# Performance work log

Hardware: AMD Instinct MI355X
Metric: run time of the kernel (lower is better)

The kernel has to match this reference:

```python
import jax, jax.numpy as jnp
import numpy as np

B, C, HZ, HX = 32, 256, 13, 25

# ---------- basic layers ----------

def _conv1x1(x, w, b):
    # x: [B,Cin,H,W], w: [Cout,Cin]
    return jnp.einsum('bchw,oc->bohw', x, w) + b[None, :, None, None]

def _conv2d(x, w, b, pad):
    y = jax.lax.conv_general_dilated(x, w, (1, 1), [(pad, pad), (pad, pad)],
                                     dimension_numbers=('NCHW', 'OIHW', 'NCHW'))
    return y + b[None, :, None, None]

def _bn(x, gamma, beta, mean, var):
    # eval-mode batchnorm with running stats, eps=1e-5 (torch default)
    s = gamma / jnp.sqrt(var + 1e-5)
    return x * s[None, :, None, None] + (beta - mean * s)[None, :, None, None]

def _gelu(x):
    return jax.nn.gelu(x, approximate=False)  # torch nn.GELU default = exact erf

# ---------- sparsemax (softThresholdingOperation) ----------
# The torch topk version recursively refines unresolved rows with 2*topk; since
# 2*128>=169 and 2*512>=625 it is mathematically exact sparsemax here.

def _sparsemax_impl(s):
    s = s - jnp.max(s, axis=-1, keepdims=True)
    d = s.shape[-1]
    z = -jnp.sort(-s, axis=-1)                      # descending sort
    cs = jnp.cumsum(z, axis=-1) - 1.0
    k = jnp.arange(1, d + 1, dtype=s.dtype)
    support = k * z > cs
    supp = jnp.sum(support, axis=-1, keepdims=True)  # int support size
    tau = jnp.take_along_axis(cs, supp - 1, axis=-1) / supp.astype(s.dtype)
    out = jnp.maximum(s - tau, 0.0)
    return out, (out, supp)

@jax.custom_vjp
def sparsemax(s):
    return _sparsemax_impl(s)[0]

def _sm_fwd(s):
    return _sparsemax_impl(s)

def _sm_bwd(res, g):
    out, supp = res
    gi = jnp.where(out != 0, g, 0.0)
    v_hat = jnp.sum(gi, axis=-1, keepdims=True) / supp.astype(out.dtype)
    return (jnp.where(out != 0, gi - v_hat, gi),)

sparsemax.defvjp(_sm_fwd, _sm_bwd)

# ---------- connected components + fill holes (GPU-native, no scipy) ----------

def _dilate8_max(lab):
    # 3x3 max-pool label propagation (8-connectivity, matches np.ones((3,3)))
    Bb, H, W = lab.shape
    p = jnp.pad(lab, ((0, 0), (1, 1), (1, 1)))
    shifts = [p[:, i:i + H, j:j + W] for i in range(3) for j in range(3)]
    return jnp.max(jnp.stack(shifts, 0), 0)

def _dilate4_or(x):
    # cross-shaped binary dilation (4-connectivity, scipy fill_holes default)
    Bb, H, W = x.shape
    p = jnp.pad(x, ((0, 0), (1, 1), (1, 1)))
    return (p[:, 1:H + 1, 1:W + 1] | p[:, 0:H, 1:W + 1] | p[:, 2:H + 2, 1:W + 1]
            | p[:, 1:H + 1, 0:W] | p[:, 1:H + 1, 2:W + 2])

def _largest_cc_filled(m):
    # m: bool [B,H,W] -> float mask of largest 8-connected component, holes filled
    Bb, H, W = m.shape
    HW = H * W
    idx = jnp.arange(1, HW + 1, dtype=jnp.int32).reshape(1, H, W)
    lab0 = jnp.where(m, idx, 0)

    def body(st):
        lab, _ = st
        return (jnp.where(m, _dilate8_max(lab), 0), lab)

    lab = jax.lax.while_loop(lambda st: jnp.any(st[0] != st[1]), body,
                             (lab0, -jnp.ones_like(lab0)))[0]

    counts = jax.vmap(lambda l, mm: jnp.zeros(HW + 1, jnp.int32)
                      .at[l.ravel()].add(mm.ravel()))(lab, m.astype(jnp.int32))
    largest = jnp.argmax(counts.at[:, 0].set(-1), axis=-1).astype(jnp.int32)
    comp = (lab == largest[:, None, None]) & m

    # fill holes: flood-fill background (4-conn) from the border, invert
    bg = ~comp
    border = jnp.zeros((H, W), bool).at[0].set(True).at[-1].set(True) \
        .at[:, 0].set(True).at[:, -1].set(True)
    seed = bg & border[None]

    def body2(st):
        r, _ = st
        return (bg & _dilate4_or(r), r)

    reach = jax.lax.while_loop(lambda st: jnp.any(st[0] != st[1]), body2,
                               (seed, jnp.zeros_like(seed)))[0]
    return ~reach

# ---------- module forward ----------

def _forward(zf, xf, sup_w, sup_b, sup_gamma, sup_beta, sup_mean, sup_var,
             q_w, q_b, q_gamma, q_beta, q_mean, q_var,
             g_w1, g_b1, g_w2, g_b2, g_gamma, g_beta, g_mean, g_var,
             fi_w, fi_b, fi_gamma, fi_beta, fi_mean, fi_var,
             fi1_w, fi1_b, fi1_gamma, fi1_beta, fi1_mean, fi1_var):
    Bb, Cc, Hz, Wz = zf.shape
    _, _, Hx, Wx = xf.shape

    xf_trans = _gelu(_bn(_conv1x1(xf, q_w, q_b), q_gamma, q_beta, q_mean, q_var))
    zf_trans = _gelu(_bn(_conv1x1(zf, sup_w, sup_b), sup_gamma, sup_beta, sup_mean, sup_var))
    xf_g = _gelu(_bn(_conv1x1(_conv2d(xf, g_w1, g_b1, 1), g_w2, g_b2),
                     g_gamma, g_beta, g_mean, g_var))

    zt = zf_trans.reshape(Bb, Cc, Hz * Wz)
    xt = xf_trans.reshape(Bb, Cc, Hx * Wx)
    zp = zf.reshape(Bb, Cc, Hz * Wz)
    xp = xf.reshape(Bb, Cc, Hx * Wx)

    zf_s = sparsemax(jnp.einsum('bcn,bcm->bnm', zt, zt))      # [B,169,169]
    zp = zp + jnp.einsum('bcn,bnm->bcm', zp, zf_s)

    si = sparsemax(jnp.einsum('bcn,bcm->bnm', zp, xp))         # [B,169,625]
    si2 = sparsemax(jnp.einsum('bcn,bcm->bnm', zp, xt))
    si = si + si2

    mask2 = jax.lax.stop_gradient(jnp.mean(si2, axis=1)) != 0  # [B,625]
    mask = _largest_cc_filled(mask2.reshape(Bb, Hx, Wx)).astype(xf.dtype)[:, None]

    si_img = si.reshape(Bb, Hz * Wz, Hx, Wx)                   # [B,169,25,25]
    fi_out = _gelu(_bn(_conv1x1(si_img, fi_w, fi_b), fi_gamma, fi_beta, fi_mean, fi_var))
    concat = jnp.concatenate([fi_out, xf_g * mask], axis=1)
    return _gelu(_bn(_conv2d(concat, fi1_w, fi1_b, 2),
                     fi1_gamma, fi1_beta, fi1_mean, fi1_var))

# ---------- setup ----------

def setup_inputs() -> dict:
    key = jax.random.key(0)
    ks = jax.random.split(key, 40)
    f32 = jnp.float32

    def n(k, shape, s=0.05):
        return (jax.random.normal(k, shape) * s).astype(f32)

    inp = {}
    inp['zf'] = jax.random.normal(ks[0], (B, C, HZ, HZ), f32)
    inp['xf'] = jax.random.normal(ks[1], (B, C, HX, HX), f32)

    def bn_params(pfx, k0):
        inp[pfx + '_gamma'] = (1.0 + n(ks[k0], (C,))).astype(f32)
        inp[pfx + '_beta'] = n(ks[k0 + 1], (C,))
        inp[pfx + '_mean'] = n(ks[k0 + 2], (C,))
        inp[pfx + '_var'] = jax.random.uniform(ks[k0 + 3], (C,), f32, 0.5, 1.5)

    inp['sup_w'] = n(ks[2], (C, C), 0.06); inp['sup_b'] = n(ks[3], (C,))
    bn_params('sup', 4)
    inp['q_w'] = n(ks[8], (C, C), 0.06); inp['q_b'] = n(ks[9], (C,))
    bn_params('q', 10)
    inp['g_w1'] = n(ks[14], (C, C, 3, 3), 0.02); inp['g_b1'] = n(ks[15], (C,))
    inp['g_w2'] = n(ks[16], (C, C), 0.06); inp['g_b2'] = n(ks[17], (C,))
    bn_params('g', 18)
    inp['fi_w'] = n(ks[22], (C, HZ * HZ), 0.08); inp['fi_b'] = n(ks[23], (C,))
    bn_params('fi', 24)
    inp['fi1_w'] = n(ks[28], (C, 2 * C, 5, 5), 0.01); inp['fi1_b'] = n(ks[29], (C,))
    bn_params('fi1', 30)
    return inp


def reference(zf, xf, sup_w, sup_b, sup_gamma, sup_beta, sup_mean, sup_var,
              q_w, q_b, q_gamma, q_beta, q_mean, q_var,
              g_w1, g_b1, g_w2, g_b2, g_gamma, g_beta, g_mean, g_var,
              fi_w, fi_b, fi_gamma, fi_beta, fi_mean, fi_var,
              fi1_w, fi1_b, fi1_gamma, fi1_beta, fi1_mean, fi1_var):
    return _forward(zf, xf, sup_w, sup_b, sup_gamma, sup_beta, sup_mean, sup_var,
                    q_w, q_b, q_gamma, q_beta, q_mean, q_var,
                    g_w1, g_b1, g_w2, g_b2, g_gamma, g_beta, g_mean, g_var,
                    fi_w, fi_b, fi_gamma, fi_beta, fi_mean, fi_var,
                    fi1_w, fi1_b, fi1_gamma, fi1_beta, fi1_mean, fi1_var)
```

## Files before the change

### kernel.cpp

```cpp
#include <hip/hip_runtime.h>
#include <hip/hip_bf16.h>
#include <math.h>

#define BB  32
#define CC  256
#define NZ  169
#define NX  625

typedef _Float16 f16x4 __attribute__((ext_vector_type(4)));
typedef _Float16 f16x8 __attribute__((ext_vector_type(8)));
typedef float    f32x4 __attribute__((ext_vector_type(4)));

__device__ __forceinline__ float geluf(float x) {
  return 0.5f * x * (1.0f + erff(x * 0.7071067811865476f));
}

struct GP {
  const float* A;  const float* B;
  const float* bias; const float* gamma; const float* beta; const float* mean; const float* var;
  const float* resid;
  float* out;
  int M, N, K;
  long aB, bB, outB;
};

#define TM 64
#define TN 64
#define TK 16

template<int AG, int EPI>
__global__ __launch_bounds__(256) void gemm_k(GP p) {
  const int b  = blockIdx.z;
  const int m0 = blockIdx.y * TM;
  const int n0 = blockIdx.x * TN;
  const float* Ab = p.A + (size_t)b * p.aB;
  const float* Bb = p.B + (size_t)b * p.bB;
  __shared__ __align__(16) float As[TK][TM + 4];
  __shared__ __align__(16) float Bs[TK][TN + 4];
  const int tid = threadIdx.x;
  const int tx = tid & 15, ty = tid >> 4;
  float acc[4][4] = {{0.f}};
  const int nK = (p.K + TK - 1) / TK;
  for (int kb = 0; kb < nK; ++kb) {
    const int k0 = kb * TK;
    if (AG == 0) {
      #pragma unroll
      for (int i = 0; i < 4; ++i) {
        int e = tid * 4 + i;
        int am = e >> 4, ak = e & 15;
        int gm = m0 + am, gk = k0 + ak;
        float v = 0.f;
        if (gm < p.M && gk < p.K) v = Ab[(size_t)gm * p.K + gk];
        As[ak][am] = v;
      }
    } else {
      #pragma unroll
      for (int i = 0; i < 4; ++i) {
        int e = tid + 256 * i;
        int ak = e >> 6, am = e & 63;
        int gm = m0 + am, gk = k0 + ak;
        float v = 0.f;
        if (gm < p.M && gk < p.K) v = Ab[(size_t)gk * p.M + gm];
        As[ak][am] = v;
      }
    }
    #pragma unroll
    for (int i = 0; i < 4; ++i) {
      int e = tid + 256 * i;
      int bk = e >> 6, bn = e & 63;
      int gk = k0 + bk, gn = n0 + bn;
      float v = 0.f;
      if (gk < p.K && gn < p.N) v = Bb[(size_t)gk * p.N + gn];
      Bs[bk][bn] = v;
    }
    __syncthreads();
    #pragma unroll
    for (int kk = 0; kk < TK; ++kk) {
      float av[4], bv[4];
      #pragma unroll
      for (int i2 = 0; i2 < 4; ++i2) av[i2] = As[kk][ty * 4 + i2];
      #pragma unroll
      for (int j2 = 0; j2 < 4; ++j2) bv[j2] = Bs[kk][tx * 4 + j2];
      #pragma unroll
      for (int i2 = 0; i2 < 4; ++i2)
        #pragma unroll
        for (int j2 = 0; j2 < 4; ++j2)
          acc[i2][j2] = fmaf(av[i2], bv[j2], acc[i2][j2]);
    }
    __syncthreads();
  }
  #pragma unroll
  for (int i = 0; i < 4; ++i) {
    int gm = m0 + ty * 4 + i;
    if (gm >= p.M) continue;
    float bs = 0.f, sBN = 1.f, tBN = 0.f;
    if (EPI == 2) {
      bs = p.bias[gm];
      float sc = p.gamma[gm] / sqrtf(p.var[gm] + 1e-5f);
      sBN = sc; tBN = p.beta[gm] - p.mean[gm] * sc;
    }
    #pragma unroll
    for (int j = 0; j < 4; ++j) {
      int gn = n0 + tx * 4 + j;
      if (gn >= p.N) continue;
      float v = acc[i][j];
      if (EPI == 2) { v += bs; v = v * sBN + tBN; v = geluf(v); }
      if (EPI == 3) v += p.resid[(size_t)b * p.outB + (size_t)gm * p.N + gn];
      p.out[(size_t)b * p.outB + (size_t)gm * p.N + gn] = v;
    }
  }
}

__global__ __launch_bounds__(256) void wtr_k(const float* __restrict__ W,
                                             _Float16* __restrict__ Wt,
                                             int M, int C2, int C2p, int R) {
  size_t o = (size_t)blockIdx.x * 256 + threadIdx.x;
  size_t total = (size_t)R * M * C2p;
  if (o >= total) return;
  int c = (int)(o % C2p);
  int t = (int)(o / C2p);
  int m = t % M;
  int r = t / M;
  float v = 0.f;
  if (c < C2) v = W[((size_t)m * C2 + c) * R + r];
  Wt[o] = (_Float16)v;
}

__global__ __launch_bounds__(256) void cvt_k(const float* __restrict__ A,
                                             const float* __restrict__ A2,
                                             _Float16* __restrict__ O,
                                             int C, int Cp, long total) {
  long o = (long)blockIdx.x * 256 + threadIdx.x;
  if (o >= total) return;
  int c = (int)(o % Cp);
  long t = o / Cp;
  int pp = (int)(t % NX);
  int b = (int)(t / NX);
  float v = 0.f;
  if (c < C) {
    size_t src = ((size_t)b * C + c) * NX + pp;
    v = A[src];
    if (A2) v += A2[src];
  }
  O[o] = (_Float16)v;
}

struct MP {
  const _Float16* Wt;
  const _Float16* U;
  const float* mask;
  const float* bias; const float* gamma; const float* beta; const float* mean; const float* var;
  float* out;
  _Float16* out16;
  int R, Rw, C2p;
  long uB;
  int oC2p, oCoff;
};

template<int EPI, int OUT16, int MASKED>
__global__ __launch_bounds__(256) void mgemm_k(MP p) {
  const int L   = blockIdx.x + 10 * (blockIdx.y + 4 * blockIdx.z);
  const int xcd = L & 7;
  const int j   = L >> 3;
  const int jb  = j / 40;
  const int b   = (xcd << 2) + jb;
  const int t   = j - jb * 40;
  const int m0  = (t / 10) * 64;
  const int n0  = (t - (t / 10) * 10) * 64;

  __shared__ __align__(16) _Float16 As[64][64];
  __shared__ __align__(16) _Float16 Bs[64][64];
  const int tid = threadIdx.x;
  const int w = tid >> 6, lane = tid & 63;
  const int wm = w & 1, wn = w >> 1;
  const int lm = lane & 15, q = lane >> 4;
  const int sr = tid >> 2, sc4 = tid & 3;
  const int scc = sc4 * 16;
  const int sr7 = sr & 7, sb = sc4 * 2;
  const int ng = n0 + sr;
  const bool nv = ng < NX;
  const int py = ng / 25, px = ng - (ng / 25) * 25;
  const _Float16* Ub = p.U + (size_t)b * p.uB;
  const float* mb = MASKED ? (p.mask + (size_t)b * NX) : nullptr;
  const int pad = p.Rw >> 1;

  f32x4 acc[2][2] = {};

  for (int r = 0; r < p.R; ++r) {
    const int kh = r / p.Rw, kw = r - (r / p.Rw) * p.Rw;
    const int iy = py + kh - pad, ix = px + kw - pad;
    const bool pv = nv && ((unsigned)iy < 25u) && ((unsigned)ix < 25u);
    const int pp = iy * 25 + ix;
    const _Float16* Up = pv ? (Ub + (size_t)pp * p.C2p) : nullptr;
    _Float16 mh = (_Float16)1.f;
    if (MASKED && pv) mh = (_Float16)mb[pp];
    const _Float16* Wr = p.Wt + ((size_t)r * 256 + m0) * p.C2p;
    for (int c0 = 0; c0 < p.C2p; c0 += 64) {
      const _Float16* Arow = Wr + (size_t)sr * p.C2p + c0 + scc;
      f16x8 a0 = *(const f16x8*)(Arow);
      f16x8 a1 = *(const f16x8*)(Arow + 8);
      f16x8 v0 = {}, v1 = {};
      if (pv) {
        const _Float16* Bp = Up + c0 + scc;
        v0 = *(const f16x8*)(Bp);
        v1 = *(const f16x8*)(Bp + 8);
        if (MASKED && (c0 + scc) >= 256) { v0 = v0 * mh; v1 = v1 * mh; }
      }
      *(f16x8*)&As[sr][((sb + 0) ^ sr7) << 3] = a0;
      *(f16x8*)&As[sr][((sb + 1) ^ sr7) << 3] = a1;
      *(f16x8*)&Bs[sr][((sb + 0) ^ sr7) << 3] = v0;
      *(f16x8*)&Bs[sr][((sb + 1) ^ sr7) << 3] = v1;
      __syncthreads();
      #pragma unroll
      for (int ks = 0; ks < 2; ++ks) {
        const int so = (((ks << 2) + q) ^ (lm & 7)) << 3;
        f16x8 af[2], bf[2];
        #pragma unroll
        for (int fm = 0; fm < 2; ++fm)
          af[fm] = *(const f16x8*)&As[wm * 32 + fm * 16 + lm][so];
        #pragma unroll
        for (int fn = 0; fn < 2; ++fn)
          bf[fn] = *(const f16x8*)&Bs[wn * 32 + fn * 16 + lm][so];
        #pragma unroll
        for (int fm = 0; fm < 2; ++fm)
          #pragma unroll
          for (int fn = 0; fn < 2; ++fn)
            acc[fm][fn] = __builtin_amdgcn_mfma_f32_16x16x32_f16(
                af[fm], bf[fn], acc[fm][fn], 0, 0, 0);
      }
      __syncthreads();
    }
  }
  #pragma unroll
  for (int fm = 0; fm < 2; ++fm) {
    const int rbase = m0 + wm * 32 + fm * 16 + q * 4;
    #pragma unroll
    for (int rr = 0; rr < 4; ++rr) {
      const int row = rbase + rr;
      float bs = p.bias[row];
      float sBN = 1.f, tBN = 0.f;
      if (EPI == 2) {
        float sc = p.gamma[row] / sqrtf(p.var[row] + 1e-5f);
        sBN = sc; tBN = p.beta[row] - p.mean[row] * sc;
      }
      #pragma unroll
      for (int fn = 0; fn < 2; ++fn) {
        const int col = n0 + wn * 32 + fn * 16 + lm;
        if (col < NX) {
          float v = acc[fm][fn][rr] + bs;
          if (EPI == 2) v = geluf(v * sBN + tBN);
          if (OUT16) {
            p.out16[((size_t)b * NX + col) * p.oC2p + p.oCoff + row] = (_Float16)v;
          } else {
            p.out[(size_t)b * (256 * NX) + (size_t)row * NX + col] = v;
          }
        }
      }
    }
  }
}

__global__ __launch_bounds__(256) void sparsemax_k(float* __restrict__ S, int d) {
  const int row = blockIdx.x;
  float* s = S + (size_t)row * d;
  const int tid = threadIdx.x;
  const int wid = tid >> 6, lane = tid & 63;
  float v[3]; bool act[3];
  #pragma unroll
  for (int j = 0; j < 3; ++j) {
    int idx = tid + j * 256;
    bool ok = idx < d;
    v[j] = ok ? s[idx] : -1e30f;
    act[j] = ok;
  }
  __shared__ float red[16];
  float mx = fmaxf(fmaxf(v[0], v[1]), v[2]);
  #pragma unroll
  for (int o = 32; o; o >>= 1) mx = fmaxf(mx, __shfl_down(mx, o));
  if (lane == 0) red[wid] = mx;
  __syncthreads();
  if (tid == 0) red[0] = fmaxf(fmaxf(red[0], red[1]), fmaxf(red[2], red[3]));
  __syncthreads();
  mx = red[0];
  __syncthreads();
  #pragma unroll
  for (int j = 0; j < 3; ++j) if (act[j]) v[j] -= mx;
  float tau = 0.f;
  for (int it = 0; it < 700; ++it) {
    float ls = 0.f, lc = 0.f;
    #pragma unroll
    for (int j = 0; j < 3; ++j) if (act[j]) { ls += v[j]; lc += 1.f; }
    #pragma unroll
    for (int o = 32; o; o >>= 1) { ls += __shfl_down(ls, o); lc += __shfl_down(lc, o); }
    if (lane == 0) { red[wid] = ls; red[4 + wid] = lc; }
    __syncthreads();
    if (tid == 0) {
      float Sm = 0.f, Cn = 0.f;
      #pragma unroll
      for (int w2 = 0; w2 < 4; ++w2) { Sm += red[w2]; Cn += red[4 + w2]; }
      red[8] = (Sm - 1.f) / Cn;
      red[9] = 0.f;
    }
    __syncthreads();
    tau = red[8];
    bool ch = false;
    #pragma unroll
    for (int j = 0; j < 3; ++j)
      if (act[j] && v[j] <= tau) { act[j] = false; ch = true; }
    if (ch) red[9] = 1.f;
    __syncthreads();
    if (red[9] == 0.f) break;
  }
  #pragma unroll
  for (int j = 0; j < 3; ++j) {
    int idx = tid + j * 256;
    if (idx < d) s[idx] = fmaxf(v[j] - tau, 0.f);
  }
}

__global__ __launch_bounds__(640) void cc_kernel(const float* __restrict__ si2,
                                                 float* __restrict__ mask) {
  const int b = blockIdx.x, tid = threadIdx.x;
  __shared__ int lab[625];
  __shared__ int counts[626];
  __shared__ int flag, best;
  const bool in = tid < 625;
  const int y = tid / 25, x = tid - (tid / 25) * 25;
  bool mv = false;
  if (in) {
    const float* base = si2 + (size_t)b * NZ * NX + tid;
    for (int n = 0; n < NZ; ++n) mv = mv || (base[(size_t)n * NX] > 0.f);
    lab[tid] = mv ? tid + 1 : 0;
  }
  __syncthreads();
  for (int it = 0; it < 1000; ++it) {
    if (tid == 0) flag = 0;
    __syncthreads();
    int nl = 0;
    if (in && mv) {
      nl = lab[tid];
      #pragma unroll
      for (int dy = -1; dy <= 1; ++dy)
        #pragma unroll
        for (int dx = -1; dx <= 1; ++dx) {
          int yy = y + dy, xx = x + dx;
          if ((unsigned)yy < 25u && (unsigned)xx < 25u) nl = max(nl, lab[yy * 25 + xx]);
        }
    }
    __syncthreads();
    if (in && mv && nl != lab[tid]) { lab[tid] = nl; flag = 1; }
    __syncthreads();
    if (flag == 0) break;
  }
  if (tid < 626) counts[tid] = (tid == 0) ? -1 : 0;
  if (tid == 0) best = (int)0x80000000;
  __syncthreads();
  if (in && mv) atomicAdd(&counts[lab[tid]], 1);
  __syncthreads();
  if (tid < 626) atomicMax(&best, counts[tid] * 1024 + (1023 - tid));
  __syncthreads();
  const int largest = 1023 - (best & 1023);
  const bool comp = in && mv && (lab[tid] == largest);
  const bool bg = in && !comp;
  const bool border = in && (y == 0 || y == 24 || x == 0 || x == 24);
  __syncthreads();
  if (in) lab[tid] = (bg && border) ? 1 : 0;
  __syncthreads();
  for (int it = 0; it < 1000; ++it) {
    if (tid == 0) flag = 0;
    __syncthreads();
    int r = 0;
    if (in && bg && !lab[tid]) {
      if (y > 0  && lab[tid - 25]) r = 1;
      if (y < 24 && lab[tid + 25]) r = 1;
      if (x > 0  && lab[tid - 1])  r = 1;
      if (x < 24 && lab[tid + 1])  r = 1;
    }
    __syncthreads();
    if (r) { lab[tid] = 1; flag = 1; }
    __syncthreads();
    if (flag == 0) break;
  }
  if (in) mask[(size_t)b * NX + tid] = lab[tid] ? 0.f : 1.f;
}

extern "C" void kernel_launch(void* const* d_in, const int* in_sizes, int n_in,
                              void* d_out, int out_size, void* d_ws, size_t ws_size,
                              hipStream_t stream) {
  const float* zf     = (const float*)d_in[0];
  const float* xf     = (const float*)d_in[1];
  const float* sup_w  = (const float*)d_in[2];
  const float* sup_b  = (const float*)d_in[3];
  const float* sup_g  = (const float*)d_in[4];
  const float* sup_be = (const float*)d_in[5];
  const float* sup_m  = (const float*)d_in[6];
  const float* sup_v  = (const float*)d_in[7];
  const float* q_w    = (const float*)d_in[8];
  const float* q_b    = (const float*)d_in[9];
  const float* q_g    = (const float*)d_in[10];
  const float* q_be   = (const float*)d_in[11];
  const float* q_m    = (const float*)d_in[12];
  const float* q_v    = (const float*)d_in[13];
  const float* g_w1   = (const float*)d_in[14];
  const float* g_b1   = (const float*)d_in[15];
  const float* g_w2   = (const float*)d_in[16];
  const float* g_b2   = (const float*)d_in[17];
  const float* g_g    = (const float*)d_in[18];
  const float* g_be   = (const float*)d_in[19];
  const float* g_m    = (const float*)d_in[20];
  const float* g_v    = (const float*)d_in[21];
  const float* fi_w   = (const float*)d_in[22];
  const float* fi_b   = (const float*)d_in[23];
  const float* fi_g   = (const float*)d_in[24];
  const float* fi_be  = (const float*)d_in[25];
  const float* fi_m   = (const float*)d_in[26];
  const float* fi_v   = (const float*)d_in[27];
  const float* fi1_w  = (const float*)d_in[28];
  const float* fi1_b  = (const float*)d_in[29];
  const float* fi1_g  = (const float*)d_in[30];
  const float* fi1_be = (const float*)d_in[31];
  const float* fi1_m  = (const float*)d_in[32];
  const float* fi1_v  = (const float*)d_in[33];

  float* ws = (float*)d_ws;
  float* xf_trans = ws;
  float* zf_trans = xf_trans + 5120000;
  float* zf_s     = zf_trans + 1384448;
  float* zp2      = zf_s + 913952;
  float* si       = zp2 + 1384448;
  float* si2      = si + 3380000;
  float* maskb    = si2 + 3380000;
  float* tail     = maskb + 20000;

  _Float16* xf16 = (_Float16*)tail;
  _Float16* gt16 = xf16 + 5120000;
  _Float16* Ucat = gt16 + 5120000;
  _Float16* S16  = Ucat + 10240000;

  _Float16* wt_g1  = (_Float16*)xf_trans;
  _Float16* wt_g2  = wt_g1 + 589824;
  _Float16* wt_fi  = wt_g2 + 65536;
  _Float16* wt_fi1 = wt_fi + 49152;

  dim3 blk(256);
  GP p;

  p = GP{}; p.A = q_w; p.B = xf; p.bias = q_b;
  p.gamma = q_g; p.beta = q_be; p.mean = q_m; p.var = q_v;
  p.out = xf_trans; p.M = CC; p.N = NX; p.K = CC;
  p.aB = 0; p.bB = (long)CC * NX; p.outB = (long)CC * NX;
  gemm_k<0,2><<<dim3(10,4,BB), blk, 0, stream>>>(p);

  p = GP{}; p.A = sup_w; p.B = zf; p.bias = sup_b;
  p.gamma = sup_g; p.beta = sup_be; p.mean = sup_m; p.var = sup_v;
  p.out = zf_trans; p.M = CC; p.N = NZ; p.K = CC;
  p.aB = 0; p.bB = (long)CC * NZ; p.outB = (long)CC * NZ;
  gemm_k<0,2><<<dim3(3,4,BB), blk, 0, stream>>>(p);

  p = GP{}; p.A = zf_trans; p.B = zf_trans;
  p.out = zf_s; p.M = NZ; p.N = NZ; p.K = CC;
  p.aB = (long)CC * NZ; p.bB = (long)CC * NZ; p.outB = (long)NZ * NZ;
  gemm_k<1,0><<<dim3(3,3,BB), blk, 0, stream>>>(p);

  sparsemax_k<<<BB * NZ, blk, 0, stream>>>(zf_s, NZ);

  p = GP{}; p.A = zf; p.B = zf_s; p.resid = zf;
  p.out = zp2; p.M = CC; p.N = NZ; p.K = NZ;
  p.aB = (long)CC * NZ; p.bB = (long)NZ * NZ; p.outB = (long)CC * NZ;
  gemm_k<0,3><<<dim3(3,4,BB), blk, 0, stream>>>(p);

  p = GP{}; p.A = zp2; p.B = xf;
  p.out = si; p.M = NZ; p.N = NX; p.K = CC;
  p.aB = (long)CC * NZ; p.bB = (long)CC * NX; p.outB = (long)NZ * NX;
  gemm_k<1,0><<<dim3(10,3,BB), blk, 0, stream>>>(p);

  p = GP{}; p.A = zp2; p.B = xf_trans;
  p.out = si2; p.M = NZ; p.N = NX; p.K = CC;
  p.aB = (long)CC * NZ; p.bB = (long)CC * NX; p.outB = (long)NZ * NX;
  gemm_k<1,0><<<dim3(10,3,BB), blk, 0, stream>>>(p);

  sparsemax_k<<<2 * BB * NZ, blk, 0, stream>>>(si, NX);

  cc_kernel<<<BB, dim3(640), 0, stream>>>(si2, maskb);

  wtr_k<<<(9*256*256 + 255)/256,  blk, 0, stream>>>(g_w1,  wt_g1,  256, 256, 256, 9);
  wtr_k<<<(256*256   + 255)/256,  blk, 0, stream>>>(g_w2,  wt_g2,  256, 256, 256, 1);
  wtr_k<<<(256*192   + 255)/256,  blk, 0, stream>>>(fi_w,  wt_fi,  256, 169, 192, 1);
  wtr_k<<<(25*256*512+ 255)/256,  blk, 0, stream>>>(fi1_w, wt_fi1, 256, 512, 512, 25);

  cvt_k<<<(long)(BB*NX*256 + 255)/256, blk, 0, stream>>>(xf, nullptr, xf16, 256, 256, (long)BB*NX*256);
  cvt_k<<<(long)(BB*NX*192 + 255)/256, blk, 0, stream>>>(si, si2, S16, 169, 192, (long)BB*NX*192);

  MP mp;

  mp = MP{}; mp.Wt = wt_g1; mp.U = xf16; mp.bias = g_b1;
  mp.out16 = gt16; mp.R = 9; mp.Rw = 3; mp.C2p = 256;
  mp.uB = (long)NX * 256; mp.oC2p = 256; mp.oCoff = 0;
  mgemm_k<1,1,0><<<dim3(10,4,BB), blk, 0, stream>>>(mp);

  mp = MP{}; mp.Wt = wt_g2; mp.U = gt16; mp.bias = g_b2;
  mp.gamma = g_g; mp.beta = g_be; mp.mean = g_m; mp.var = g_v;
  mp.out16 = Ucat; mp.R = 1; mp.Rw = 1; mp.C2p = 256;
  mp.uB = (long)NX * 256; mp.oC2p = 512; mp.oCoff = 256;
  mgemm_k<2,1,0><<<dim3(10,4,BB), blk, 0, stream>>>(mp);

  mp = MP{}; mp.Wt = wt_fi; mp.U = S16; mp.bias = fi_b;
  mp.gamma = fi_g; mp.beta = fi_be; mp.mean = fi_m; mp.var = fi_v;
  mp.out16 = Ucat; mp.R = 1; mp.Rw = 1; mp.C2p = 192;
  mp.uB = (long)NX * 192; mp.oC2p = 512; mp.oCoff = 0;
  mgemm_k<2,1,0><<<dim3(10,4,BB), blk, 0, stream>>>(mp);

  mp = MP{}; mp.Wt = wt_fi1; mp.U = Ucat; mp.mask = maskb;
  mp.bias = fi1_b; mp.gamma = fi1_g; mp.beta = fi1_be; mp.mean = fi1_m; mp.var = fi1_v;
  mp.out = (float*)d_out; mp.R = 25; mp.Rw = 5; mp.C2p = 512;
  mp.uB = (long)NX * 512;
  mgemm_k<2,0,1><<<dim3(10,4,BB), blk, 0, stream>>>(mp);
}
```

Baseline: 867.6 us.

## Double-buffer LDS tiles in mgemm with register prefetch of next K-tile

The mgemm kernel now uses two LDS buffers and a flattened K loop. The next tile's global loads go into registers while MFMAs run on the current buffer, which leaves one barrier per iteration. This is meant to hide global-load latency behind compute. To fit the power-of-two channel-tile indexing, the fi GEMM pads its channels from 192 to 256. That adds some wasted zero-padded work and doubles the shared memory per block, which may reduce occupancy.

```diff
diff --git a/kernel.cpp b/kernel.cpp
--- a/kernel.cpp
+++ b/kernel.cpp
@@ -168,8 +168,8 @@
   const int m0  = (t / 10) * 64;
   const int n0  = (t - (t / 10) * 10) * 64;
 
-  __shared__ __align__(16) _Float16 As[64][64];
-  __shared__ __align__(16) _Float16 Bs[64][64];
+  __shared__ __align__(16) _Float16 As[2][64][64];
+  __shared__ __align__(16) _Float16 Bs[2][64][64];
   const int tid = threadIdx.x;
   const int w = tid >> 6, lane = tid & 63;
   const int wm = w & 1, wn = w >> 1;
@@ -183,54 +183,70 @@
   const _Float16* Ub = p.U + (size_t)b * p.uB;
   const float* mb = MASKED ? (p.mask + (size_t)b * NX) : nullptr;
   const int pad = p.Rw >> 1;
+  const int cSh = (p.C2p == 512) ? 3 : 2;
+  const int cMask = (1 << cSh) - 1;
+  const int KT = p.R << cSh;
 
   f32x4 acc[2][2] = {};
-
-  for (int r = 0; r < p.R; ++r) {
+  f16x8 a0, a1, v0, v1;
+
+  auto LOADIT = [&](int kt) {
+    const int r  = kt >> cSh;
+    const int c0 = (kt & cMask) << 6;
     const int kh = r / p.Rw, kw = r - (r / p.Rw) * p.Rw;
     const int iy = py + kh - pad, ix = px + kw - pad;
     const bool pv = nv && ((unsigned)iy < 25u) && ((unsigned)ix < 25u);
     const int pp = iy * 25 + ix;
-    const _Float16* Up = pv ? (Ub + (size_t)pp * p.C2p) : nullptr;
-    _Float16 mh = (_Float16)1.f;
-    if (MASKED && pv) mh = (_Float16)mb[pp];
-    const _Float16* Wr = p.Wt + ((size_t)r * 256 + m0) * p.C2p;
-    for (int c0 = 0; c0 < p.C2p; c0 += 64) {
-      const _Float16* Arow = Wr + (size_t)sr * p.C2p + c0 + scc;
-      f16x8 a0 = *(const f16x8*)(Arow);
-      f16x8 a1 = *(const f16x8*)(Arow + 8);
-      f16x8 v0 = {}, v1 = {};
-      if (pv) {
-        const _Float16* Bp = Up + c0 + scc;
-        v0 = *(const f16x8*)(Bp);
-        v1 = *(const f16x8*)(Bp + 8);
-        if (MASKED && (c0 + scc) >= 256) { v0 = v0 * mh; v1 = v1 * mh; }
+    const _Float16* Arow = p.Wt + ((size_t)r * 256 + m0 + sr) * p.C2p + c0 + scc;
+    a0 = *(const f16x8*)(Arow);
+    a1 = *(const f16x8*)(Arow + 8);
+    v0 = {}; v1 = {};
+    if (pv) {
+      const _Float16* Bp = Ub + (size_t)pp * p.C2p + c0 + scc;
+      v0 = *(const f16x8*)(Bp);
+      v1 = *(const f16x8*)(Bp + 8);
+      if (MASKED && (c0 + scc) >= 256) {
+        _Float16 mh = (_Float16)mb[pp];
+        v0 = v0 * mh; v1 = v1 * mh;
       }
-      *(f16x8*)&As[sr][((sb + 0) ^ sr7) << 3] = a0;
-      *(f16x8*)&As[sr][((sb + 1) ^ sr7) << 3] = a1;
-      *(f16x8*)&Bs[sr][((sb + 0) ^ sr7) << 3] = v0;
-      *(f16x8*)&Bs[sr][((sb + 1) ^ sr7) << 3] = v1;
-      __syncthreads();
-      #pragma unroll
-      for (int ks = 0; ks < 2; ++ks) {
-        const int so = (((ks << 2) + q) ^ (lm & 7)) << 3;
-        f16x8 af[2], bf[2];
-        #pragma unroll
-        for (int fm = 0; fm < 2; ++fm)
-          af[fm] = *(const f16x8*)&As[wm * 32 + fm * 16 + lm][so];
+    }
+  };
+  auto STORE = [&](int buf) {
+    *(f16x8*)&As[buf][sr][((sb + 0) ^ sr7) << 3] = a0;
+    *(f16x8*)&As[buf][sr][((sb + 1) ^ sr7) << 3] = a1;
+    *(f16x8*)&Bs[buf][sr][((sb + 0) ^ sr7) << 3] = v0;
+    *(f16x8*)&Bs[buf][sr][((sb + 1) ^ sr7) << 3] = v1;
+  };
+
+  LOADIT(0);
+  STORE(0);
+  __syncthreads();
+
+  for (int kt = 0; kt < KT; ++kt) {
+    const int cur = kt & 1;
+    const bool more = (kt + 1 < KT);
+    if (more) LOADIT(kt + 1);
+    #pragma unroll
+    for (int ks = 0; ks < 2; ++ks) {
+      const int so = (((ks << 2) + q) ^ (lm & 7)) << 3;
+      f16x8 af[2], bf[2];
+      #pragma unroll
+      for (int fm = 0; fm < 2; ++fm)
+        af[fm] = *(const f16x8*)&As[cur][wm * 32 + fm * 16 + lm][so];
+      #pragma unroll
+      for (int fn = 0; fn < 2; ++fn)
+        bf[fn] = *(const f16x8*)&Bs[cur][wn * 32 + fn * 16 + lm][so];
+      #pragma unroll
+      for (int fm = 0; fm < 2; ++fm)
         #pragma unroll
         for (int fn = 0; fn < 2; ++fn)
-          bf[fn] = *(const f16x8*)&Bs[wn * 32 + fn * 16 + lm][so];
-        #pragma unroll
-        for (int fm = 0; fm < 2; ++fm)
-          #pragma unroll
-          for (int fn = 0; fn < 2; ++fn)
-            acc[fm][fn] = __builtin_amdgcn_mfma_f32_16x16x32_f16(
-                af[fm], bf[fn], acc[fm][fn], 0, 0, 0);
-      }
-      __syncthreads();
-    }
-  }
+          acc[fm][fn] = __builtin_amdgcn_mfma_f32_16x16x32_f16(
+              af[fm], bf[fn], acc[fm][fn], 0, 0, 0);
+    }
+    if (more) STORE(cur ^ 1);
+    __syncthreads();
+  }
+
   #pragma unroll
   for (int fm = 0; fm < 2; ++fm) {
     const int rbase = m0 + wm * 32 + fm * 16 + q * 4;
@@ -440,7 +456,7 @@
   _Float16* wt_g1  = (_Float16*)xf_trans;
   _Float16* wt_g2  = wt_g1 + 589824;
   _Float16* wt_fi  = wt_g2 + 65536;
-  _Float16* wt_fi1 = wt_fi + 49152;
+  _Float16* wt_fi1 = wt_fi + 65536;
 
   dim3 blk(256);
   GP p;
@@ -485,11 +501,11 @@
 
   wtr_k<<<(9*256*256 + 255)/256,  blk, 0, stream>>>(g_w1,  wt_g1,  256, 256, 256, 9);
   wtr_k<<<(256*256   + 255)/256,  blk, 0, stream>>>(g_w2,  wt_g2,  256, 256, 256, 1);
-  wtr_k<<<(256*192   + 255)/256,  blk, 0, stream>>>(fi_w,  wt_fi,  256, 169, 192, 1);
+  wtr_k<<<(256*256   + 255)/256,  blk, 0, stream>>>(fi_w,  wt_fi,  256, 169, 256, 1);
   wtr_k<<<(25*256*512+ 255)/256,  blk, 0, stream>>>(fi1_w, wt_fi1, 256, 512, 512, 25);
 
   cvt_k<<<(long)(BB*NX*256 + 255)/256, blk, 0, stream>>>(xf, nullptr, xf16, 256, 256, (long)BB*NX*256);
-  cvt_k<<<(long)(BB*NX*192 + 255)/256, blk, 0, stream>>>(si, si2, S16, 169, 192, (long)BB*NX*192);
+  cvt_k<<<(long)(BB*NX*256 + 255)/256, blk, 0, stream>>>(si, si2, S16, 169, 256, (long)BB*NX*256);
 
   MP mp;
 
@@ -506,8 +522,8 @@
 
   mp = MP{}; mp.Wt = wt_fi; mp.U = S16; mp.bias = fi_b;
   mp.gamma = fi_g; mp.beta = fi_be; mp.mean = fi_m; mp.var = fi_v;
-  mp.out16 = Ucat; mp.R = 1; mp.Rw = 1; mp.C2p = 192;
-  mp.uB = (long)NX * 192; mp.oC2p = 512; mp.oCoff = 0;
+  mp.out16 = Ucat; mp.R = 1; mp.Rw = 1; mp.C2p = 256;
+  mp.uB = (long)NX * 256; mp.oC2p = 512; mp.oCoff = 0;
   mgemm_k<2,1,0><<<dim3(10,4,BB), blk, 0, stream>>>(mp);
 
   mp = MP{}; mp.Wt = wt_fi1; mp.U = Ucat; mp.mask = maskb;
```

Measured after the change: 944.9 us. +8.9%, slower.
